# Kernel optimization log

Measured on AMD Instinct MI355X. Metric: run time of the kernel, lower is better.

Reference implementation:

```python
import jax, jax.numpy as jnp
import numpy as np

TEMPERATURE = 0.07
EPS = 1e-12  # F.normalize eps


def setup_inputs() -> dict:
    key = jax.random.key(0)
    k1, k2 = jax.random.split(key)
    B, D = 4096, 1024
    return {
        "features_1": jax.random.normal(k1, (B, D), dtype=jnp.float32),
        "features_2": jax.random.normal(k2, (B, D), dtype=jnp.float32),
    }


def _l2_normalize(x):
    n = jnp.sqrt(jnp.sum(x * x, axis=1, keepdims=True))
    return x / jnp.maximum(n, EPS)


def reference(features_1, features_2):
    B = features_1.shape[0]
    f1 = _l2_normalize(features_1)
    f2 = _l2_normalize(features_2)
    f = jnp.concatenate([f1, f2], axis=0)  # [2B, D]
    # cosine sim of already-normalized vectors == plain matmul
    sim = (f @ f.T) / TEMPERATURE  # [2B, 2B]
    # denominator: logsumexp over each row excluding the diagonal (self-sim)
    eye = jnp.eye(2 * B, dtype=bool)
    lse = jax.nn.logsumexp(jnp.where(eye, -jnp.inf, sim), axis=1)  # [2B]
    # positives: cross-view pairs (i+B, i) then (i, i+B)
    idx = jnp.arange(B)
    pos = jnp.concatenate([sim[idx + B, idx], sim[idx, idx + B]], axis=0)  # [2B]
    loss = -jnp.mean(pos - lse)
    return loss
```

## Files before the change

kernel.cpp:

```cpp
#include <hip/hip_runtime.h>
#include <hip/hip_bf16.h>
#include <math.h>

#define INV_T (1.0f / 0.07f)

typedef float f32x4 __attribute__((ext_vector_type(4)));
typedef long lx2 __attribute__((ext_vector_type(2)));

__device__ __forceinline__ void gld16(const void* g, void* l) {
    __builtin_amdgcn_global_load_lds(
        (const __attribute__((address_space(1))) unsigned int*)g,
        (__attribute__((address_space(3))) unsigned int*)l,
        16, 0, 0);
}

__global__ __launch_bounds__(256) void norm_kernel(
    const float4* __restrict__ f1, const float4* __restrict__ f2,
    unsigned int* __restrict__ F, float* __restrict__ S, float* __restrict__ P,
    unsigned int* __restrict__ cnt, int B) {
    const int i = blockIdx.x;
    const int t = threadIdx.x;

    float4 x = f1[(size_t)i * 256 + t];
    float4 y = f2[(size_t)i * 256 + t];

    float s1 = x.x * x.x + x.y * x.y + x.z * x.z + x.w * x.w;
    float s2 = y.x * y.x + y.y * y.y + y.z * y.z + y.w * y.w;
    float dd = x.x * y.x + x.y * y.y + x.z * y.z + x.w * y.w;

    for (int o = 32; o > 0; o >>= 1) {
        s1 += __shfl_down(s1, o);
        s2 += __shfl_down(s2, o);
        dd += __shfl_down(dd, o);
    }
    __shared__ float red[4][3];
    const int wv = t >> 6, ln = t & 63;
    if (ln == 0) { red[wv][0] = s1; red[wv][1] = s2; red[wv][2] = dd; }
    __syncthreads();
    s1 = red[0][0] + red[1][0] + red[2][0] + red[3][0];
    s2 = red[0][1] + red[1][1] + red[2][1] + red[3][1];
    dd = red[0][2] + red[1][2] + red[2][2] + red[3][2];

    const float rn1 = 1.0f / fmaxf(sqrtf(s1), 1e-12f);
    const float rn2 = 1.0f / fmaxf(sqrtf(s2), 1e-12f);

    unsigned int w1 = __builtin_amdgcn_cvt_pk_fp8_f32(x.x * rn1, x.y * rn1, 0, 0);
    w1 = __builtin_amdgcn_cvt_pk_fp8_f32(x.z * rn1, x.w * rn1, w1, 1);
    F[(size_t)i * 256 + t] = w1;
    unsigned int w2 = __builtin_amdgcn_cvt_pk_fp8_f32(y.x * rn2, y.y * rn2, 0, 0);
    w2 = __builtin_amdgcn_cvt_pk_fp8_f32(y.z * rn2, y.w * rn2, w2, 1);
    F[(size_t)(B + i) * 256 + t] = w2;

    if (t == 0) {
        P[i] = dd * rn1 * rn2;
        S[i] = 0.0f;
        S[B + i] = 0.0f;
        if (i == 0) { cnt[0] = 0u; cnt[1] = 0u; }
    }
}

__global__ __launch_bounds__(256, 2) void sim_kernel(
    const unsigned char* __restrict__ F, float* __restrict__ S,
    const float* __restrict__ P, unsigned int* __restrict__ cnt,
    float* __restrict__ out, int N, int D, int B, int NT) {
    __shared__ __align__(16) unsigned char As[128][128];
    __shared__ __align__(16) unsigned char Bs[256][128];
    __shared__ int kShared;

    const int tid  = threadIdx.x;
    const int wave = tid >> 6;
    const int lane = tid & 63;
    const int quad = lane >> 4;
    const int l16  = lane & 15;

    const int srow   = lane >> 3;
    const int ldsOff = (lane & 7) * 16;
    const int srcOff = ((lane & 7) ^ srow) * 16;

    const int waveRow = (wave >> 1) * 64;
    const int waveCol = (wave & 1) * 128;

    while (true) {
        if (tid == 0) kShared = (int)atomicAdd(&cnt[1], 1u);
        __syncthreads();
        const int k = kShared;
        if (k >= NT) break;

        int tj = (int)((sqrtf(4.0f * (float)k + 1.0f) - 1.0f) * 0.5f);
        while ((tj + 1) * (tj + 2) <= k) ++tj;
        while (tj * (tj + 1) > k) --tj;
        const int ti = k - tj * (tj + 1);
        const int bRow = ti * 128;
        const int bCol = tj * 256;

        f32x4 acc[4][8];
#pragma unroll
        for (int mi = 0; mi < 4; ++mi)
#pragma unroll
            for (int ni = 0; ni < 8; ++ni)
                acc[mi][ni] = (f32x4){0.0f, 0.0f, 0.0f, 0.0f};

        for (int kb = 0; kb < D; kb += 128) {
#pragma unroll
            for (int p = 0; p < 4; ++p) {
                const int rowT = (p * 4 + wave) * 8 + srow;
                gld16(&F[(size_t)(bRow + rowT) * D + kb + srcOff], &As[rowT][ldsOff]);
            }
#pragma unroll
            for (int p = 0; p < 8; ++p) {
                const int rowT = (p * 4 + wave) * 8 + srow;
                gld16(&F[(size_t)(bCol + rowT) * D + kb + srcOff], &Bs[rowT][ldsOff]);
            }
            __syncthreads();

#pragma unroll
            for (int hf = 0; hf < 2; ++hf) {
                lx2 bfr[8];
#pragma unroll
                for (int ni = 0; ni < 8; ++ni) {
                    const int r = waveCol + ni * 16 + l16;
                    bfr[ni] = *(const lx2*)&Bs[r][(((quad << 1) | hf) ^ (r & 7)) * 16];
                }
                lx2 afr[4];
#pragma unroll
                for (int mi = 0; mi < 4; ++mi) {
                    const int r = waveRow + mi * 16 + l16;
                    afr[mi] = *(const lx2*)&As[r][(((quad << 1) | hf) ^ (r & 7)) * 16];
                }
#pragma unroll
                for (int mi = 0; mi < 4; ++mi)
#pragma unroll
                    for (int ni = 0; ni < 8; ++ni) {
                        acc[mi][ni] = __builtin_amdgcn_mfma_f32_16x16x32_fp8_fp8(
                            afr[mi].x, bfr[ni].x, acc[mi][ni], 0, 0, 0);
                        acc[mi][ni] = __builtin_amdgcn_mfma_f32_16x16x32_fp8_fp8(
                            afr[mi].y, bfr[ni].y, acc[mi][ni], 0, 0, 0);
                    }
            }
            __syncthreads();
        }

#pragma unroll
        for (int mi = 0; mi < 4; ++mi)
#pragma unroll
            for (int ni = 0; ni < 8; ++ni)
#pragma unroll
                for (int r = 0; r < 4; ++r) {
                    const int gRow = bRow + waveRow + mi * 16 + quad * 4 + r;
                    const int gCol = bCol + waveCol + ni * 16 + l16;
                    acc[mi][ni][r] = (gRow < gCol)
                        ? __expf((acc[mi][ni][r] - 1.0f) * INV_T) : 0.0f;
                }

#pragma unroll
        for (int mi = 0; mi < 4; ++mi)
#pragma unroll
            for (int r = 0; r < 4; ++r) {
                const int gRow = bRow + waveRow + mi * 16 + quad * 4 + r;
                float v = 0.0f;
#pragma unroll
                for (int ni = 0; ni < 8; ++ni) v += acc[mi][ni][r];
                v += __shfl_xor(v, 1);
                v += __shfl_xor(v, 2);
                v += __shfl_xor(v, 4);
                v += __shfl_xor(v, 8);
                if (l16 == 0) atomicAdd(&S[gRow], v);
            }

#pragma unroll
        for (int ni = 0; ni < 8; ++ni) {
            float cv = 0.0f;
#pragma unroll
            for (int mi = 0; mi < 4; ++mi)
#pragma unroll
                for (int r = 0; r < 4; ++r) cv += acc[mi][ni][r];
            cv += __shfl_xor(cv, 16);
            cv += __shfl_xor(cv, 32);
            if (quad == 0) atomicAdd(&S[bCol + waveCol + ni * 16 + l16], cv);
        }
    }

    __threadfence();
    __shared__ unsigned int ticket;
    if (tid == 0) ticket = atomicAdd(&cnt[0], 1u);
    __syncthreads();
    if (ticket == (unsigned int)(gridDim.x - 1)) {
        __threadfence();
        volatile const float* Sv = S;
        float s = 0.0f;
        for (int i = tid; i < N; i += 256) s += __logf(Sv[i]);
        float pp = 0.0f;
        for (int i = tid; i < B; i += 256) pp += P[i];
        for (int o = 32; o > 0; o >>= 1) {
            s += __shfl_down(s, o);
            pp += __shfl_down(pp, o);
        }
        __shared__ float red2[4][2];
        if ((tid & 63) == 0) { red2[tid >> 6][0] = s; red2[tid >> 6][1] = pp; }
        __syncthreads();
        if (tid == 0) {
            const float sl = red2[0][0] + red2[1][0] + red2[2][0] + red2[3][0];
            const float ps = red2[0][1] + red2[1][1] + red2[2][1] + red2[3][1];
            out[0] = INV_T + sl / (float)N - ps * (2.0f * INV_T / (float)N);
        }
    }
}

extern "C" void kernel_launch(void* const* d_in, const int* in_sizes, int n_in,
                              void* d_out, int out_size, void* d_ws, size_t ws_size,
                              hipStream_t stream) {
    const int D = 1024;
    const int B = in_sizes[0] / D;
    const int N = 2 * B;
    const int M2 = N / 256;
    const int NT = M2 * M2 + M2;

    const float* f1 = (const float*)d_in[0];
    const float* f2 = (const float*)d_in[1];

    unsigned char* F = (unsigned char*)d_ws;
    float* S = (float*)(F + (size_t)N * D);
    float* P = S + N;
    unsigned int* cnt = (unsigned int*)(P + B);

    norm_kernel<<<dim3(B), dim3(256), 0, stream>>>(
        (const float4*)f1, (const float4*)f2, (unsigned int*)F, S, P, cnt, B);
    sim_kernel<<<dim3(512), dim3(256), 0, stream>>>(
        F, S, P, cnt, (float*)d_out, N, D, B, NT);
}
```

Baseline: 192.8 us.

## Replace persistent work queue with one 256x256 triangular tile per block

Drops the persistent atomic work-queue loop. Each block now handles one 256x256 upper-triangular tile of the similarity matrix with 512 threads (8 waves), so the grid is M(M+1)/2 blocks. The larger square tile gives more operand reuse per byte loaded and removes the per-tile atomic fetch. In exchange, LDS use doubles to 64KB per block and the tail is no longer load-balanced. The __launch_bounds__(512,4) hint may force a tight VGPR budget that spills the 128-float accumulator.

```diff
diff --git a/kernel.cpp b/kernel.cpp
--- a/kernel.cpp
+++ b/kernel.cpp
@@ -59,13 +59,12 @@
     }
 }
 
-__global__ __launch_bounds__(256, 2) void sim_kernel(
+__global__ __launch_bounds__(512, 4) void sim_kernel(
     const unsigned char* __restrict__ F, float* __restrict__ S,
     const float* __restrict__ P, unsigned int* __restrict__ cnt,
-    float* __restrict__ out, int N, int D, int B, int NT) {
-    __shared__ __align__(16) unsigned char As[128][128];
+    float* __restrict__ out, int N, int D, int B) {
+    __shared__ __align__(16) unsigned char As[256][128];
     __shared__ __align__(16) unsigned char Bs[256][128];
-    __shared__ int kShared;
 
     const int tid  = threadIdx.x;
     const int wave = tid >> 6;
@@ -80,127 +79,122 @@
     const int waveRow = (wave >> 1) * 64;
     const int waveCol = (wave & 1) * 128;
 
-    while (true) {
-        if (tid == 0) kShared = (int)atomicAdd(&cnt[1], 1u);
+    const int k = blockIdx.x;
+    int tj = (int)((sqrtf(8.0f * (float)k + 1.0f) - 1.0f) * 0.5f);
+    while ((tj + 1) * (tj + 2) / 2 <= k) ++tj;
+    while (tj * (tj + 1) / 2 > k) --tj;
+    const int ti = k - tj * (tj + 1) / 2;
+    const int bRow = ti * 256;
+    const int bCol = tj * 256;
+
+    f32x4 acc[4][8];
+#pragma unroll
+    for (int mi = 0; mi < 4; ++mi)
+#pragma unroll
+        for (int ni = 0; ni < 8; ++ni)
+            acc[mi][ni] = (f32x4){0.0f, 0.0f, 0.0f, 0.0f};
+
+    for (int kb = 0; kb < D; kb += 128) {
+#pragma unroll
+        for (int p = 0; p < 4; ++p) {
+            const int rowT = (p * 8 + wave) * 8 + srow;
+            gld16(&F[(size_t)(bRow + rowT) * D + kb + srcOff], &As[rowT][ldsOff]);
+        }
+#pragma unroll
+        for (int p = 0; p < 4; ++p) {
+            const int rowT = (p * 8 + wave) * 8 + srow;
+            gld16(&F[(size_t)(bCol + rowT) * D + kb + srcOff], &Bs[rowT][ldsOff]);
+        }
         __syncthreads();
-        const int k = kShared;
-        if (k >= NT) break;
-
-        int tj = (int)((sqrtf(4.0f * (float)k + 1.0f) - 1.0f) * 0.5f);
-        while ((tj + 1) * (tj + 2) <= k) ++tj;
-        while (tj * (tj + 1) > k) --tj;
-        const int ti = k - tj * (tj + 1);
-        const int bRow = ti * 128;
-        const int bCol = tj * 256;
-
-        f32x4 acc[4][8];
-#pragma unroll
-        for (int mi = 0; mi < 4; ++mi)
-#pragma unroll
-            for (int ni = 0; ni < 8; ++ni)
-                acc[mi][ni] = (f32x4){0.0f, 0.0f, 0.0f, 0.0f};
-
-        for (int kb = 0; kb < D; kb += 128) {
-#pragma unroll
-            for (int p = 0; p < 4; ++p) {
-                const int rowT = (p * 4 + wave) * 8 + srow;
-                gld16(&F[(size_t)(bRow + rowT) * D + kb + srcOff], &As[rowT][ldsOff]);
+
+#pragma unroll
+        for (int hf = 0; hf < 2; ++hf) {
+            lx2 bfr[8];
+#pragma unroll
+            for (int ni = 0; ni < 8; ++ni) {
+                const int r = waveCol + ni * 16 + l16;
+                bfr[ni] = *(const lx2*)&Bs[r][(((quad << 1) | hf) ^ (r & 7)) * 16];
             }
-#pragma unroll
-            for (int p = 0; p < 8; ++p) {
-                const int rowT = (p * 4 + wave) * 8 + srow;
-                gld16(&F[(size_t)(bCol + rowT) * D + kb + srcOff], &Bs[rowT][ldsOff]);
+            lx2 afr[4];
+#pragma unroll
+            for (int mi = 0; mi < 4; ++mi) {
+                const int r = waveRow + mi * 16 + l16;
+                afr[mi] = *(const lx2*)&As[r][(((quad << 1) | hf) ^ (r & 7)) * 16];
             }
-            __syncthreads();
-
-#pragma unroll
-            for (int hf = 0; hf < 2; ++hf) {
-                lx2 bfr[8];
+#pragma unroll
+            for (int mi = 0; mi < 4; ++mi)
 #pragma unroll
                 for (int ni = 0; ni < 8; ++ni) {
-                    const int r = waveCol + ni * 16 + l16;
-                    bfr[ni] = *(const lx2*)&Bs[r][(((quad << 1) | hf) ^ (r & 7)) * 16];
+                    acc[mi][ni] = __builtin_amdgcn_mfma_f32_16x16x32_fp8_fp8(
+                        afr[mi].x, bfr[ni].x, acc[mi][ni], 0, 0, 0);
+                    acc[mi][ni] = __builtin_amdgcn_mfma_f32_16x16x32_fp8_fp8(
+                        afr[mi].y, bfr[ni].y, acc[mi][ni], 0, 0, 0);
                 }
-                lx2 afr[4];
-#pragma unroll
-                for (int mi = 0; mi < 4; ++mi) {
-                    const int r = waveRow + mi * 16 + l16;
-                    afr[mi] = *(const lx2*)&As[r][(((quad << 1) | hf) ^ (r & 7)) * 16];
-                }
-#pragma unroll
-                for (int mi = 0; mi < 4; ++mi)
-#pragma unroll
-                    for (int ni = 0; ni < 8; ++ni) {
-                        acc[mi][ni] = __builtin_amdgcn_mfma_f32_16x16x32_fp8_fp8(
-                            afr[mi].x, bfr[ni].x, acc[mi][ni], 0, 0, 0);
-                        acc[mi][ni] = __builtin_amdgcn_mfma_f32_16x16x32_fp8_fp8(
-                            afr[mi].y, bfr[ni].y, acc[mi][ni], 0, 0, 0);
-                    }
-            }
-            __syncthreads();
-        }
-
-#pragma unroll
-        for (int mi = 0; mi < 4; ++mi)
-#pragma unroll
-            for (int ni = 0; ni < 8; ++ni)
-#pragma unroll
-                for (int r = 0; r < 4; ++r) {
-                    const int gRow = bRow + waveRow + mi * 16 + quad * 4 + r;
-                    const int gCol = bCol + waveCol + ni * 16 + l16;
-                    acc[mi][ni][r] = (gRow < gCol)
-                        ? __expf((acc[mi][ni][r] - 1.0f) * INV_T) : 0.0f;
-                }
-
-#pragma unroll
-        for (int mi = 0; mi < 4; ++mi)
+        }
+        __syncthreads();
+    }
+
+#pragma unroll
+    for (int mi = 0; mi < 4; ++mi)
+#pragma unroll
+        for (int ni = 0; ni < 8; ++ni)
 #pragma unroll
             for (int r = 0; r < 4; ++r) {
                 const int gRow = bRow + waveRow + mi * 16 + quad * 4 + r;
-                float v = 0.0f;
-#pragma unroll
-                for (int ni = 0; ni < 8; ++ni) v += acc[mi][ni][r];
-                v += __shfl_xor(v, 1);
-                v += __shfl_xor(v, 2);
-                v += __shfl_xor(v, 4);
-                v += __shfl_xor(v, 8);
-                if (l16 == 0) atomicAdd(&S[gRow], v);
+                const int gCol = bCol + waveCol + ni * 16 + l16;
+                acc[mi][ni][r] = (gRow < gCol)
+                    ? __expf((acc[mi][ni][r] - 1.0f) * INV_T) : 0.0f;
             }
 
 #pragma unroll
-        for (int ni = 0; ni < 8; ++ni) {
-            float cv = 0.0f;
-#pragma unroll
-            for (int mi = 0; mi < 4; ++mi)
-#pragma unroll
-                for (int r = 0; r < 4; ++r) cv += acc[mi][ni][r];
-            cv += __shfl_xor(cv, 16);
-            cv += __shfl_xor(cv, 32);
-            if (quad == 0) atomicAdd(&S[bCol + waveCol + ni * 16 + l16], cv);
-        }
+    for (int mi = 0; mi < 4; ++mi)
+#pragma unroll
+        for (int r = 0; r < 4; ++r) {
+            const int gRow = bRow + waveRow + mi * 16 + quad * 4 + r;
+            float v = 0.0f;
+#pragma unroll
+            for (int ni = 0; ni < 8; ++ni) v += acc[mi][ni][r];
+            v += __shfl_xor(v, 1);
+            v += __shfl_xor(v, 2);
+            v += __shfl_xor(v, 4);
+            v += __shfl_xor(v, 8);
+            if (l16 == 0) atomicAdd(&S[gRow], v);
+        }
+
+#pragma unroll
+    for (int ni = 0; ni < 8; ++ni) {
+        float cv = 0.0f;
+#pragma unroll
+        for (int mi = 0; mi < 4; ++mi)
+#pragma unroll
+            for (int r = 0; r < 4; ++r) cv += acc[mi][ni][r];
+        cv += __shfl_xor(cv, 16);
+        cv += __shfl_xor(cv, 32);
+        if (quad == 0) atomicAdd(&S[bCol + waveCol + ni * 16 + l16], cv);
     }
 
     __threadfence();
-    __shared__ unsigned int ticket;
-    if (tid == 0) ticket = atomicAdd(&cnt[0], 1u);
+    volatile unsigned int* tk = (volatile unsigned int*)&As[0][0];
+    float* fin = (float*)&As[0][16];
+    if (tid == 0) *tk = atomicAdd(&cnt[0], 1u);
     __syncthreads();
-    if (ticket == (unsigned int)(gridDim.x - 1)) {
+    if (*tk == (unsigned int)(gridDim.x - 1)) {
         __threadfence();
         volatile const float* Sv = S;
         float s = 0.0f;
-        for (int i = tid; i < N; i += 256) s += __logf(Sv[i]);
+        for (int i = tid; i < N; i += 512) s += __logf(Sv[i]);
         float pp = 0.0f;
-        for (int i = tid; i < B; i += 256) pp += P[i];
+        for (int i = tid; i < B; i += 512) pp += P[i];
         for (int o = 32; o > 0; o >>= 1) {
             s += __shfl_down(s, o);
             pp += __shfl_down(pp, o);
         }
-        __shared__ float red2[4][2];
-        if ((tid & 63) == 0) { red2[tid >> 6][0] = s; red2[tid >> 6][1] = pp; }
+        if ((tid & 63) == 0) { fin[(tid >> 6) * 2] = s; fin[(tid >> 6) * 2 + 1] = pp; }
         __syncthreads();
         if (tid == 0) {
-            const float sl = red2[0][0] + red2[1][0] + red2[2][0] + red2[3][0];
-            const float ps = red2[0][1] + red2[1][1] + red2[2][1] + red2[3][1];
+            float sl = 0.0f, ps = 0.0f;
+#pragma unroll
+            for (int w = 0; w < 8; ++w) { sl += fin[w * 2]; ps += fin[w * 2 + 1]; }
             out[0] = INV_T + sl / (float)N - ps * (2.0f * INV_T / (float)N);
         }
     }
@@ -212,8 +206,8 @@
     const int D = 1024;
     const int B = in_sizes[0] / D;
     const int N = 2 * B;
-    const int M2 = N / 256;
-    const int NT = M2 * M2 + M2;
+    const int M = N / 256;
+    const int NT = M * (M + 1) / 2;
 
     const float* f1 = (const float*)d_in[0];
     const float* f2 = (const float*)d_in[1];
@@ -225,6 +219,6 @@
 
     norm_kernel<<<dim3(B), dim3(256), 0, stream>>>(
         (const float4*)f1, (const float4*)f2, (unsigned int*)F, S, P, cnt, B);
-    sim_kernel<<<dim3(512), dim3(256), 0, stream>>>(
-        F, S, P, cnt, (float*)d_out, N, D, B, NT);
-}
+    sim_kernel<<<dim3(NT), dim3(512), 0, stream>>>(
+        F, S, P, cnt, (float*)d_out, N, D, B);
+}
```

Result: slower. 691.9 us (+258.8%).
